# Kernel optimization log

Hardware: AMD Instinct MI355X
Metric: run time of the kernel (lower is better)

## Reference

```python
import jax, jax.numpy as jnp
import numpy as np

N = 4096      # nodes
IN = 512      # in_features
HEADS = 8
HPH = 8       # n_hidden // n_heads
HID = HEADS * HPH  # 64
CLS = 16      # n_classes
NEG_SLOPE = 0.2
MASK_VAL = -1e9


def setup_inputs() -> dict:
    key = jax.random.key(0)
    ks = jax.random.split(key, 8)
    x = jax.random.normal(ks[0], (N, IN), jnp.float32)
    # sparse-ish adjacency, avg degree ~16, with self loops
    adj = jax.random.bernoulli(ks[1], 16.0 / N, (N, N)) | jnp.eye(N, dtype=bool)
    W1 = jax.random.normal(ks[2], (IN, HEADS, HPH), jnp.float32) * 0.05
    a1l = jax.random.normal(ks[3], (HEADS, HPH), jnp.float32) * 0.05
    a1r = jax.random.normal(ks[4], (HEADS, HPH), jnp.float32) * 0.05
    W2 = jax.random.normal(ks[5], (HID, 1, CLS), jnp.float32) * 0.05
    a2l = jax.random.normal(ks[6], (1, CLS), jnp.float32) * 0.05
    a2r = jax.random.normal(ks[7], (1, CLS), jnp.float32) * 0.05
    return {"x": x, "adj": adj, "W1": W1, "a1l": a1l, "a1r": a1r,
            "W2": W2, "a2l": a2l, "a2r": a2r}


def gat_layer(x, adj, W, al, ar, is_concat):
    # project: [N, H, D]
    g = jnp.einsum('ni,ihd->nhd', x, W)
    # score e[i,j,h] = leaky_relu(a_l . g_i + a_r . g_j)
    sl = jnp.einsum('nhd,hd->nh', g, al)  # [N, H]
    sr = jnp.einsum('nhd,hd->nh', g, ar)  # [N, H]
    e = jax.nn.leaky_relu(sl[:, None, :] + sr[None, :, :], NEG_SLOPE)  # [N, N, H]
    e = jnp.where(adj[:, :, None], e, MASK_VAL)
    a = jax.nn.softmax(e, axis=1)                 # softmax over neighbors j
    out = jnp.einsum('ijh,jhd->ihd', a, g)        # [N, H, D]
    if is_concat:
        return out.reshape(out.shape[0], -1)      # [N, H*D]
    return out.mean(axis=1)                        # [N, D]


def reference(x, adj, W1, a1l, a1r, W2, a2l, a2r):
    # dropout layers are identity in eval mode
    h = gat_layer(x, adj, W1, a1l, a1r, True)   # [N, HID]
    h = jax.nn.elu(h)
    return gat_layer(h, adj, W2, a2l, a2r, False)  # [N, CLS]
```

## Files before the change

kernel.cpp:

```cpp
#include <hip/hip_runtime.h>
#include <hip/hip_bf16.h>

#define N_NODES 4096
#define IN_F 512
#define HEADS 8
#define HPH 8
#define HID 64
#define CLS 16
#define NEG_SLOPE 0.2f
#define MAXD 256
#define QCAP 256

__device__ __forceinline__ float leaky(float x) { return x > 0.f ? x : NEG_SLOPE * x; }

__global__ __launch_bounds__(256, 4) void scan_proj1(
        const int* __restrict__ adj,
        const float* __restrict__ x,
        const float* __restrict__ W1,
        const float* __restrict__ a1l,
        const float* __restrict__ a1r,
        float* __restrict__ g1,
        float* __restrict__ sl1,
        float* __restrict__ sr1,
        int* __restrict__ deg_g,
        int* __restrict__ nbr_g) {
    __shared__ float xs[16][516];
    __shared__ int wcnt[4];
    const int b = blockIdx.x;
    const int t = threadIdx.x;
    const int group = b / 17;
    const int role = b - group * 17;
    if (role < 16) {
        int* nbrS = (int*)&xs[0][0];
        const int w = t >> 6, lane = t & 63;
        const int i = group * 16 + role;
        const int4* q = (const int4*)(adj + (size_t)i * N_NODES) + w * 256;
        const int4 v0 = q[lane];
        const int4 v1 = q[lane + 64];
        const int4 v2 = q[lane + 128];
        const int4 v3 = q[lane + 192];
        const unsigned long long below = (1ull << lane) - 1ull;
        int* seg = nbrS + w * QCAP;
        const int jq = w * 1024;
        int segcnt = 0;
        {
            const int4 v = v0; const int s = 0;
            const bool fx = v.x != 0, fy = v.y != 0, fz = v.z != 0, fw = v.w != 0;
            const unsigned long long bx = __ballot(fx), by = __ballot(fy);
            const unsigned long long bz = __ballot(fz), bw = __ballot(fw);
            int base = segcnt + __popcll(bx & below) + __popcll(by & below)
                              + __popcll(bz & below) + __popcll(bw & below);
            const int j0 = jq + 4 * (lane + 64 * s);
            int r = 0;
            if (fx) { if (base + r < QCAP) seg[base + r] = j0;     ++r; }
            if (fy) { if (base + r < QCAP) seg[base + r] = j0 + 1; ++r; }
            if (fz) { if (base + r < QCAP) seg[base + r] = j0 + 2; ++r; }
            if (fw) { if (base + r < QCAP) seg[base + r] = j0 + 3; ++r; }
            segcnt += __popcll(bx) + __popcll(by) + __popcll(bz) + __popcll(bw);
        }
        {
            const int4 v = v1; const int s = 1;
            const bool fx = v.x != 0, fy = v.y != 0, fz = v.z != 0, fw = v.w != 0;
            const unsigned long long bx = __ballot(fx), by = __ballot(fy);
            const unsigned long long bz = __ballot(fz), bw = __ballot(fw);
            int base = segcnt + __popcll(bx & below) + __popcll(by & below)
                              + __popcll(bz & below) + __popcll(bw & below);
            const int j0 = jq + 4 * (lane + 64 * s);
            int r = 0;
            if (fx) { if (base + r < QCAP) seg[base + r] = j0;     ++r; }
            if (fy) { if (base + r < QCAP) seg[base + r] = j0 + 1; ++r; }
            if (fz) { if (base + r < QCAP) seg[base + r] = j0 + 2; ++r; }
            if (fw) { if (base + r < QCAP) seg[base + r] = j0 + 3; ++r; }
            segcnt += __popcll(bx) + __popcll(by) + __popcll(bz) + __popcll(bw);
        }
        {
            const int4 v = v2; const int s = 2;
            const bool fx = v.x != 0, fy = v.y != 0, fz = v.z != 0, fw = v.w != 0;
            const unsigned long long bx = __ballot(fx), by = __ballot(fy);
            const unsigned long long bz = __ballot(fz), bw = __ballot(fw);
            int base = segcnt + __popcll(bx & below) + __popcll(by & below)
                              + __popcll(bz & below) + __popcll(bw & below);
            const int j0 = jq + 4 * (lane + 64 * s);
            int r = 0;
            if (fx) { if (base + r < QCAP) seg[base + r] = j0;     ++r; }
            if (fy) { if (base + r < QCAP) seg[base + r] = j0 + 1; ++r; }
            if (fz) { if (base + r < QCAP) seg[base + r] = j0 + 2; ++r; }
            if (fw) { if (base + r < QCAP) seg[base + r] = j0 + 3; ++r; }
            segcnt += __popcll(bx) + __popcll(by) + __popcll(bz) + __popcll(bw);
        }
        {
            const int4 v = v3; const int s = 3;
            const bool fx = v.x != 0, fy = v.y != 0, fz = v.z != 0, fw = v.w != 0;
            const unsigned long long bx = __ballot(fx), by = __ballot(fy);
            const unsigned long long bz = __ballot(fz), bw = __ballot(fw);
            int base = segcnt + __popcll(bx & below) + __popcll(by & below)
                              + __popcll(bz & below) + __popcll(bw & below);
            const int j0 = jq + 4 * (lane + 64 * s);
            int r = 0;
            if (fx) { if (base + r < QCAP) seg[base + r] = j0;     ++r; }
            if (fy) { if (base + r < QCAP) seg[base + r] = j0 + 1; ++r; }
            if (fz) { if (base + r < QCAP) seg[base + r] = j0 + 2; ++r; }
            if (fw) { if (base + r < QCAP) seg[base + r] = j0 + 3; ++r; }
            segcnt += __popcll(bx) + __popcll(by) + __popcll(bz) + __popcll(bw);
        }
        const int myc = segcnt < QCAP ? segcnt : QCAP;
        if (lane == 0) wcnt[w] = myc;
        __syncthreads();
        const int off = (w > 0 ? wcnt[0] : 0) + (w > 1 ? wcnt[1] : 0)
                      + (w > 2 ? wcnt[2] : 0);
        const int total = wcnt[0] + wcnt[1] + wcnt[2] + wcnt[3];
        if (t == 0) deg_g[i] = total < MAXD ? total : MAXD;
        for (int k = lane; k < myc; k += 64) {
            const int pos = off + k;
            if (pos < MAXD) nbr_g[(size_t)i * MAXD + pos] = seg[k];
        }
        return;
    }
    const int i0 = group * 16;
    for (int l = t; l < 2048; l += 256) {
        const int r = l >> 7, c4 = l & 127;
        *(float4*)&xs[r][c4 * 4] = *(const float4*)(x + (size_t)(i0 + r) * IN_F + c4 * 4);
    }
    __syncthreads();
    const int wv = t >> 6;
    const int inner = t & 63;
    const int kq = inner >> 4;
    const int cg = inner & 15;
    float4 acc[4];
#pragma unroll
    for (int r = 0; r < 4; ++r) acc[r] = make_float4(0.f, 0.f, 0.f, 0.f);
    const float* xr[4];
#pragma unroll
    for (int r = 0; r < 4; ++r) xr[r] = &xs[wv * 4 + r][kq * 128];
    const float* Wq = W1 + (size_t)(kq * 128) * HID + cg * 4;
#pragma unroll 2
    for (int k = 0; k < 128; k += 4) {
        const float4 w0 = *(const float4*)(Wq + (size_t)(k + 0) * HID);
        const float4 w1 = *(const float4*)(Wq + (size_t)(k + 1) * HID);
        const float4 w2 = *(const float4*)(Wq + (size_t)(k + 2) * HID);
        const float4 w3 = *(const float4*)(Wq + (size_t)(k + 3) * HID);
#pragma unroll
        for (int r = 0; r < 4; ++r) {
            const float4 xv = *(const float4*)(xr[r] + k);
            acc[r].x += xv.x * w0.x + xv.y * w1.x + xv.z * w2.x + xv.w * w3.x;
            acc[r].y += xv.x * w0.y + xv.y * w1.y + xv.z * w2.y + xv.w * w3.y;
            acc[r].z += xv.x * w0.z + xv.y * w1.z + xv.z * w2.z + xv.w * w3.z;
            acc[r].w += xv.x * w0.w + xv.y * w1.w + xv.z * w2.w + xv.w * w3.w;
        }
    }
#pragma unroll
    for (int r = 0; r < 4; ++r) {
#pragma unroll
        for (int m = 16; m <= 32; m <<= 1) {
            acc[r].x += __shfl_xor(acc[r].x, m, 64);
            acc[r].y += __shfl_xor(acc[r].y, m, 64);
            acc[r].z += __shfl_xor(acc[r].z, m, 64);
            acc[r].w += __shfl_xor(acc[r].w, m, 64);
        }
    }
    if (kq == 0) {
        const float4 al = *(const float4*)(a1l + cg * 4);
        const float4 ar = *(const float4*)(a1r + cg * 4);
#pragma unroll
        for (int r = 0; r < 4; ++r) {
            const int i = i0 + wv * 4 + r;
            *(float4*)(g1 + (size_t)i * HID + cg * 4) = acc[r];
            float pl = acc[r].x * al.x + acc[r].y * al.y + acc[r].z * al.z + acc[r].w * al.w;
            float pr = acc[r].x * ar.x + acc[r].y * ar.y + acc[r].z * ar.z + acc[r].w * ar.w;
            pl += __shfl_xor(pl, 1, 64);
            pr += __shfl_xor(pr, 1, 64);
            if ((cg & 1) == 0) {
                sl1[i * HEADS + (cg >> 1)] = pl;
                sr1[i * HEADS + (cg >> 1)] = pr;
            }
        }
    }
}

__global__ __launch_bounds__(256) void attn1_fused(
        const float* __restrict__ g1,
        const float* __restrict__ sl1,
        const float* __restrict__ sr1,
        const float* __restrict__ W2,
        const float* __restrict__ a2l,
        const float* __restrict__ a2r,
        const int* __restrict__ deg_g,
        const int* __restrict__ nbr_g,
        float* __restrict__ g2,
        float* __restrict__ sl2,
        float* __restrict__ sr2) {
    const int w = threadIdx.x >> 6;
    const int t = threadIdx.x & 63;
    const int i = blockIdx.x * 4 + w;
    const int n = deg_g[i];
    const int jreg = nbr_g[(size_t)i * MAXD + t];
    const int h = t >> 3;
    const float sl = sl1[i * HEADS + h];
    float denom = 0.f, acc = 0.f;
    const int n64 = n < 64 ? n : 64;
    int k = 0;
    for (; k + 4 <= n64; k += 4) {
        const int j0 = __shfl(jreg, k),     j1 = __shfl(jreg, k + 1);
        const int j2 = __shfl(jreg, k + 2), j3 = __shfl(jreg, k + 3);
        const float s0 = sr1[j0 * HEADS + h], s1 = sr1[j1 * HEADS + h];
        const float s2 = sr1[j2 * HEADS + h], s3 = sr1[j3 * HEADS + h];
        const float v0 = g1[(size_t)j0 * HID + t], v1 = g1[(size_t)j1 * HID + t];
        const float v2 = g1[(size_t)j2 * HID + t], v3 = g1[(size_t)j3 * HID + t];
        const float w0 = __expf(leaky(sl + s0)), w1 = __expf(leaky(sl + s1));
        const float w2 = __expf(leaky(sl + s2)), w3 = __expf(leaky(sl + s3));
        denom += (w0 + w1) + (w2 + w3);
        acc += w0 * v0; acc += w1 * v1; acc += w2 * v2; acc += w3 * v3;
    }
    for (; k < n64; ++k) {
        const int jj = __shfl(jreg, k);
        const float wq = __expf(leaky(sl + sr1[jj * HEADS + h]));
        denom += wq;
        acc += wq * g1[(size_t)jj * HID + t];
    }
    for (; k < n; ++k) {
        const int jj = nbr_g[(size_t)i * MAXD + k];
        const float wq = __expf(leaky(sl + sr1[jj * HEADS + h]));
        denom += wq;
        acc += wq * g1[(size_t)jj * HID + t];
    }
    float o = (n > 0) ? (acc / denom) : 0.f;
    o = (o > 0.f) ? o : expm1f(o);
    const int q = t >> 4, c = t & 15;
    float p = 0.f;
#pragma unroll
    for (int kk = 0; kk < 16; ++kk) {
        const int k2 = q * 16 + kk;
        p += __shfl(o, k2) * W2[k2 * CLS + c];
    }
    p += __shfl_xor(p, 16, 64);
    p += __shfl_xor(p, 32, 64);
    float pl = 0.f, pr = 0.f;
    if (t < CLS) {
        g2[(size_t)i * CLS + t] = p;
        pl = p * a2l[t];
        pr = p * a2r[t];
    }
#pragma unroll
    for (int off = 1; off < 16; off <<= 1) {
        pl += __shfl_xor(pl, off, 64);
        pr += __shfl_xor(pr, off, 64);
    }
    if (t == 0) { sl2[i] = pl; sr2[i] = pr; }
}

__global__ __launch_bounds__(256) void attn2(
        const int* __restrict__ deg_g,
        const int* __restrict__ nbr_g,
        const float* __restrict__ g2,
        const float* __restrict__ sl2,
        const float* __restrict__ sr2,
        float* __restrict__ out) {
    const int w = threadIdx.x >> 6;
    const int t = threadIdx.x & 63;
    const int g = t >> 4;
    const int c = t & 15;
    const int node = blockIdx.x * 16 + w * 4 + g;
    const int n = deg_g[node];
    const int4 jv = *(const int4*)(nbr_g + (size_t)node * MAXD + 4 * c);
    const float sl = sl2[node];
    float denom = 0.f, acc = 0.f;
    const int n64 = n < 64 ? n : 64;
    int k = 0;
    for (; k + 4 <= n64; k += 4) {
        const int src = k >> 2;
        const int j0 = __shfl(jv.x, src, 16), j1 = __shfl(jv.y, src, 16);
        const int j2 = __shfl(jv.z, src, 16), j3 = __shfl(jv.w, src, 16);
        const float s0 = sr2[j0], s1 = sr2[j1], s2 = sr2[j2], s3 = sr2[j3];
        const float v0 = g2[(size_t)j0 * CLS + c], v1 = g2[(size_t)j1 * CLS + c];
        const float v2 = g2[(size_t)j2 * CLS + c], v3 = g2[(size_t)j3 * CLS + c];
        const float w0 = __expf(leaky(sl + s0)), w1 = __expf(leaky(sl + s1));
        const float w2 = __expf(leaky(sl + s2)), w3 = __expf(leaky(sl + s3));
        denom += (w0 + w1) + (w2 + w3);
        acc += w0 * v0; acc += w1 * v1; acc += w2 * v2; acc += w3 * v3;
    }
    for (; k < n64; ++k) {
        const int src = k >> 2, cm = k & 3;
        const int jx = __shfl(jv.x, src, 16), jy = __shfl(jv.y, src, 16);
        const int jz = __shfl(jv.z, src, 16), jw = __shfl(jv.w, src, 16);
        const int jj = cm == 0 ? jx : (cm == 1 ? jy : (cm == 2 ? jz : jw));
        const float wq = __expf(leaky(sl + sr2[jj]));
        denom += wq;
        acc += wq * g2[(size_t)jj * CLS + c];
    }
    for (; k < n; ++k) {
        const int jj = nbr_g[(size_t)node * MAXD + k];
        const float wq = __expf(leaky(sl + sr2[jj]));
        denom += wq;
        acc += wq * g2[(size_t)jj * CLS + c];
    }
    out[(size_t)node * CLS + c] = (n > 0) ? acc / denom : 0.f;
}

extern "C" void kernel_launch(void* const* d_in, const int* in_sizes, int n_in,
                              void* d_out, int out_size, void* d_ws, size_t ws_size,
                              hipStream_t stream) {
    const float* x   = (const float*)d_in[0];
    const int*   adj = (const int*)d_in[1];
    const float* W1  = (const float*)d_in[2];
    const float* a1l = (const float*)d_in[3];
    const float* a1r = (const float*)d_in[4];
    const float* W2  = (const float*)d_in[5];
    const float* a2l = (const float*)d_in[6];
    const float* a2r = (const float*)d_in[7];
    float* out = (float*)d_out;

    float* ws  = (float*)d_ws;
    float* g1  = ws;
    float* sl1 = g1  + (size_t)N_NODES * HID;
    float* sr1 = sl1 + (size_t)N_NODES * HEADS;
    float* g2  = sr1 + (size_t)N_NODES * HEADS;
    float* sl2 = g2  + (size_t)N_NODES * CLS;
    float* sr2 = sl2 + N_NODES;
    int*   deg = (int*)(sr2 + N_NODES);
    int*   nbr = deg + N_NODES;

    scan_proj1<<<17 * (N_NODES / 16), 256, 0, stream>>>(
        adj, x, W1, a1l, a1r, g1, sl1, sr1, deg, nbr);
    attn1_fused<<<N_NODES / 4, 256, 0, stream>>>(g1, sl1, sr1, W2, a2l, a2r,
                                                 deg, nbr, g2, sl2, sr2);
    attn2<<<N_NODES / 16, 256, 0, stream>>>(deg, nbr, g2, sl2, sr2, out);
}
```

Before: 131.1 us.

## Merge three kernels into one cooperative persistent kernel with grid syncs

Replaces the three separate launches (scan+projection, layer-1 attention, layer-2 attention) with one cooperative kernel. It loops over tasks with a grid-stride and separates the stages with grid-wide syncs. The aim is to remove kernel launch gaps and inter-kernel drain/fill overhead. In exchange the grid is capped by occupancy, grid syncs add latency, and the per-node work in each stage runs over fewer resident blocks.

```diff
diff --git a/kernel.cpp b/kernel.cpp
--- a/kernel.cpp
+++ b/kernel.cpp
@@ -1,5 +1,7 @@
 #include <hip/hip_runtime.h>
-#include <hip/hip_bf16.h>
+#include <hip/hip_cooperative_groups.h>
+
+namespace cg = cooperative_groups;
 
 #define N_NODES 4096
 #define IN_F 512
@@ -10,290 +12,241 @@
 #define NEG_SLOPE 0.2f
 #define MAXD 256
 #define QCAP 256
+#define TASKS (17 * (N_NODES / 16))
 
 __device__ __forceinline__ float leaky(float x) { return x > 0.f ? x : NEG_SLOPE * x; }
 
-__global__ __launch_bounds__(256, 4) void scan_proj1(
+__device__ __forceinline__ void emit4(int4 v, int j0, int* seg, int& segcnt,
+                                      unsigned long long below) {
+    const bool fx = v.x != 0, fy = v.y != 0, fz = v.z != 0, fw = v.w != 0;
+    const unsigned long long bx = __ballot(fx), by = __ballot(fy);
+    const unsigned long long bz = __ballot(fz), bw = __ballot(fw);
+    int base = segcnt + __popcll(bx & below) + __popcll(by & below)
+                      + __popcll(bz & below) + __popcll(bw & below);
+    int r = 0;
+    if (fx) { if (base + r < QCAP) seg[base + r] = j0;     ++r; }
+    if (fy) { if (base + r < QCAP) seg[base + r] = j0 + 1; ++r; }
+    if (fz) { if (base + r < QCAP) seg[base + r] = j0 + 2; ++r; }
+    if (fw) { if (base + r < QCAP) seg[base + r] = j0 + 3; ++r; }
+    segcnt += __popcll(bx) + __popcll(by) + __popcll(bz) + __popcll(bw);
+}
+
+__global__ __launch_bounds__(256, 4) void gat_all(
         const int* __restrict__ adj,
         const float* __restrict__ x,
         const float* __restrict__ W1,
         const float* __restrict__ a1l,
         const float* __restrict__ a1r,
+        const float* __restrict__ W2,
+        const float* __restrict__ a2l,
+        const float* __restrict__ a2r,
         float* __restrict__ g1,
         float* __restrict__ sl1,
         float* __restrict__ sr1,
+        float* __restrict__ g2,
+        float* __restrict__ sl2,
+        float* __restrict__ sr2,
         int* __restrict__ deg_g,
-        int* __restrict__ nbr_g) {
+        int* __restrict__ nbr_g,
+        float* __restrict__ out) {
     __shared__ float xs[16][516];
     __shared__ int wcnt[4];
-    const int b = blockIdx.x;
     const int t = threadIdx.x;
-    const int group = b / 17;
-    const int role = b - group * 17;
-    if (role < 16) {
-        int* nbrS = (int*)&xs[0][0];
-        const int w = t >> 6, lane = t & 63;
-        const int i = group * 16 + role;
-        const int4* q = (const int4*)(adj + (size_t)i * N_NODES) + w * 256;
-        const int4 v0 = q[lane];
-        const int4 v1 = q[lane + 64];
-        const int4 v2 = q[lane + 128];
-        const int4 v3 = q[lane + 192];
-        const unsigned long long below = (1ull << lane) - 1ull;
-        int* seg = nbrS + w * QCAP;
-        const int jq = w * 1024;
-        int segcnt = 0;
-        {
-            const int4 v = v0; const int s = 0;
-            const bool fx = v.x != 0, fy = v.y != 0, fz = v.z != 0, fw = v.w != 0;
-            const unsigned long long bx = __ballot(fx), by = __ballot(fy);
-            const unsigned long long bz = __ballot(fz), bw = __ballot(fw);
-            int base = segcnt + __popcll(bx & below) + __popcll(by & below)
-                              + __popcll(bz & below) + __popcll(bw & below);
-            const int j0 = jq + 4 * (lane + 64 * s);
-            int r = 0;
-            if (fx) { if (base + r < QCAP) seg[base + r] = j0;     ++r; }
-            if (fy) { if (base + r < QCAP) seg[base + r] = j0 + 1; ++r; }
-            if (fz) { if (base + r < QCAP) seg[base + r] = j0 + 2; ++r; }
-            if (fw) { if (base + r < QCAP) seg[base + r] = j0 + 3; ++r; }
-            segcnt += __popcll(bx) + __popcll(by) + __popcll(bz) + __popcll(bw);
-        }
-        {
-            const int4 v = v1; const int s = 1;
-            const bool fx = v.x != 0, fy = v.y != 0, fz = v.z != 0, fw = v.w != 0;
-            const unsigned long long bx = __ballot(fx), by = __ballot(fy);
-            const unsigned long long bz = __ballot(fz), bw = __ballot(fw);
-            int base = segcnt + __popcll(bx & below) + __popcll(by & below)
-                              + __popcll(bz & below) + __popcll(bw & below);
-            const int j0 = jq + 4 * (lane + 64 * s);
-            int r = 0;
-            if (fx) { if (base + r < QCAP) seg[base + r] = j0;     ++r; }
-            if (fy) { if (base + r < QCAP) seg[base + r] = j0 + 1; ++r; }
-            if (fz) { if (base + r < QCAP) seg[base + r] = j0 + 2; ++r; }
-            if (fw) { if (base + r < QCAP) seg[base + r] = j0 + 3; ++r; }
-            segcnt += __popcll(bx) + __popcll(by) + __popcll(bz) + __popcll(bw);
-        }
-        {
-            const int4 v = v2; const int s = 2;
-            const bool fx = v.x != 0, fy = v.y != 0, fz = v.z != 0, fw = v.w != 0;
-            const unsigned long long bx = __ballot(fx), by = __ballot(fy);
-            const unsigned long long bz = __ballot(fz), bw = __ballot(fw);
-            int base = segcnt + __popcll(bx & below) + __popcll(by & below)
-                              + __popcll(bz & below) + __popcll(bw & below);
-            const int j0 = jq + 4 * (lane + 64 * s);
-            int r = 0;
-            if (fx) { if (base + r < QCAP) seg[base + r] = j0;     ++r; }
-            if (fy) { if (base + r < QCAP) seg[base + r] = j0 + 1; ++r; }
-            if (fz) { if (base + r < QCAP) seg[base + r] = j0 + 2; ++r; }
-            if (fw) { if (base + r < QCAP) seg[base + r] = j0 + 3; ++r; }
-            segcnt += __popcll(bx) + __popcll(by) + __popcll(bz) + __popcll(bw);
-        }
-        {
-            const int4 v = v3; const int s = 3;
-            const bool fx = v.x != 0, fy = v.y != 0, fz = v.z != 0, fw = v.w != 0;
-            const unsigned long long bx = __ballot(fx), by = __ballot(fy);
-            const unsigned long long bz = __ballot(fz), bw = __ballot(fw);
-            int base = segcnt + __popcll(bx & below) + __popcll(by & below)
-                              + __popcll(bz & below) + __popcll(bw & below);
-            const int j0 = jq + 4 * (lane + 64 * s);
-            int r = 0;
-            if (fx) { if (base + r < QCAP) seg[base + r] = j0;     ++r; }
-            if (fy) { if (base + r < QCAP) seg[base + r] = j0 + 1; ++r; }
-            if (fz) { if (base + r < QCAP) seg[base + r] = j0 + 2; ++r; }
-            if (fw) { if (base + r < QCAP) seg[base + r] = j0 + 3; ++r; }
-            segcnt += __popcll(bx) + __popcll(by) + __popcll(bz) + __popcll(bw);
-        }
-        const int myc = segcnt < QCAP ? segcnt : QCAP;
-        if (lane == 0) wcnt[w] = myc;
+    const int w = t >> 6, lane = t & 63;
+
+    for (int task = blockIdx.x; task < TASKS; task += gridDim.x) {
         __syncthreads();
-        const int off = (w > 0 ? wcnt[0] : 0) + (w > 1 ? wcnt[1] : 0)
-                      + (w > 2 ? wcnt[2] : 0);
-        const int total = wcnt[0] + wcnt[1] + wcnt[2] + wcnt[3];
-        if (t == 0) deg_g[i] = total < MAXD ? total : MAXD;
-        for (int k = lane; k < myc; k += 64) {
-            const int pos = off + k;
-            if (pos < MAXD) nbr_g[(size_t)i * MAXD + pos] = seg[k];
-        }
-        return;
-    }
-    const int i0 = group * 16;
-    for (int l = t; l < 2048; l += 256) {
-        const int r = l >> 7, c4 = l & 127;
-        *(float4*)&xs[r][c4 * 4] = *(const float4*)(x + (size_t)(i0 + r) * IN_F + c4 * 4);
-    }
-    __syncthreads();
-    const int wv = t >> 6;
-    const int inner = t & 63;
-    const int kq = inner >> 4;
-    const int cg = inner & 15;
-    float4 acc[4];
-#pragma unroll
-    for (int r = 0; r < 4; ++r) acc[r] = make_float4(0.f, 0.f, 0.f, 0.f);
-    const float* xr[4];
-#pragma unroll
-    for (int r = 0; r < 4; ++r) xr[r] = &xs[wv * 4 + r][kq * 128];
-    const float* Wq = W1 + (size_t)(kq * 128) * HID + cg * 4;
+        const int group = task / 17;
+        const int role = task - group * 17;
+        if (role < 16) {
+            int* nbrS = (int*)&xs[0][0];
+            const int i = group * 16 + role;
+            const int4* q = (const int4*)(adj + (size_t)i * N_NODES) + w * 256;
+            const int4 v0 = q[lane];
+            const int4 v1 = q[lane + 64];
+            const int4 v2 = q[lane + 128];
+            const int4 v3 = q[lane + 192];
+            const unsigned long long below = (1ull << lane) - 1ull;
+            int* seg = nbrS + w * QCAP;
+            const int jq = w * 1024;
+            int segcnt = 0;
+            emit4(v0, jq + 4 * lane, seg, segcnt, below);
+            emit4(v1, jq + 4 * (lane + 64), seg, segcnt, below);
+            emit4(v2, jq + 4 * (lane + 128), seg, segcnt, below);
+            emit4(v3, jq + 4 * (lane + 192), seg, segcnt, below);
+            const int myc = segcnt < QCAP ? segcnt : QCAP;
+            if (lane == 0) wcnt[w] = myc;
+            __syncthreads();
+            const int off = (w > 0 ? wcnt[0] : 0) + (w > 1 ? wcnt[1] : 0)
+                          + (w > 2 ? wcnt[2] : 0);
+            const int total = wcnt[0] + wcnt[1] + wcnt[2] + wcnt[3];
+            if (t == 0) deg_g[i] = total < MAXD ? total : MAXD;
+            for (int k = lane; k < myc; k += 64) {
+                const int pos = off + k;
+                if (pos < MAXD) nbr_g[(size_t)i * MAXD + pos] = seg[k];
+            }
+        } else {
+            const int i0 = group * 16;
+            for (int l = t; l < 2048; l += 256) {
+                const int r = l >> 7, c4 = l & 127;
+                *(float4*)&xs[r][c4 * 4] =
+                    *(const float4*)(x + (size_t)(i0 + r) * IN_F + c4 * 4);
+            }
+            __syncthreads();
+            const int kq = lane >> 4;
+            const int cg = lane & 15;
+            float4 acc[4];
+#pragma unroll
+            for (int r = 0; r < 4; ++r) acc[r] = make_float4(0.f, 0.f, 0.f, 0.f);
+            const float* xr[4];
+#pragma unroll
+            for (int r = 0; r < 4; ++r) xr[r] = &xs[w * 4 + r][kq * 128];
+            const float* Wq = W1 + (size_t)(kq * 128) * HID + cg * 4;
 #pragma unroll 2
-    for (int k = 0; k < 128; k += 4) {
-        const float4 w0 = *(const float4*)(Wq + (size_t)(k + 0) * HID);
-        const float4 w1 = *(const float4*)(Wq + (size_t)(k + 1) * HID);
-        const float4 w2 = *(const float4*)(Wq + (size_t)(k + 2) * HID);
-        const float4 w3 = *(const float4*)(Wq + (size_t)(k + 3) * HID);
-#pragma unroll
-        for (int r = 0; r < 4; ++r) {
-            const float4 xv = *(const float4*)(xr[r] + k);
-            acc[r].x += xv.x * w0.x + xv.y * w1.x + xv.z * w2.x + xv.w * w3.x;
-            acc[r].y += xv.x * w0.y + xv.y * w1.y + xv.z * w2.y + xv.w * w3.y;
-            acc[r].z += xv.x * w0.z + xv.y * w1.z + xv.z * w2.z + xv.w * w3.z;
-            acc[r].w += xv.x * w0.w + xv.y * w1.w + xv.z * w2.w + xv.w * w3.w;
-        }
-    }
-#pragma unroll
-    for (int r = 0; r < 4; ++r) {
-#pragma unroll
-        for (int m = 16; m <= 32; m <<= 1) {
-            acc[r].x += __shfl_xor(acc[r].x, m, 64);
-            acc[r].y += __shfl_xor(acc[r].y, m, 64);
-            acc[r].z += __shfl_xor(acc[r].z, m, 64);
-            acc[r].w += __shfl_xor(acc[r].w, m, 64);
-        }
-    }
-    if (kq == 0) {
-        const float4 al = *(const float4*)(a1l + cg * 4);
-        const float4 ar = *(const float4*)(a1r + cg * 4);
-#pragma unroll
-        for (int r = 0; r < 4; ++r) {
-            const int i = i0 + wv * 4 + r;
-            *(float4*)(g1 + (size_t)i * HID + cg * 4) = acc[r];
-            float pl = acc[r].x * al.x + acc[r].y * al.y + acc[r].z * al.z + acc[r].w * al.w;
-            float pr = acc[r].x * ar.x + acc[r].y * ar.y + acc[r].z * ar.z + acc[r].w * ar.w;
-            pl += __shfl_xor(pl, 1, 64);
-            pr += __shfl_xor(pr, 1, 64);
-            if ((cg & 1) == 0) {
-                sl1[i * HEADS + (cg >> 1)] = pl;
-                sr1[i * HEADS + (cg >> 1)] = pr;
-            }
-        }
-    }
-}
-
-__global__ __launch_bounds__(256) void attn1_fused(
-        const float* __restrict__ g1,
-        const float* __restrict__ sl1,
-        const float* __restrict__ sr1,
-        const float* __restrict__ W2,
-        const float* __restrict__ a2l,
-        const float* __restrict__ a2r,
-        const int* __restrict__ deg_g,
-        const int* __restrict__ nbr_g,
-        float* __restrict__ g2,
-        float* __restrict__ sl2,
-        float* __restrict__ sr2) {
-    const int w = threadIdx.x >> 6;
-    const int t = threadIdx.x & 63;
-    const int i = blockIdx.x * 4 + w;
-    const int n = deg_g[i];
-    const int jreg = nbr_g[(size_t)i * MAXD + t];
-    const int h = t >> 3;
-    const float sl = sl1[i * HEADS + h];
-    float denom = 0.f, acc = 0.f;
-    const int n64 = n < 64 ? n : 64;
-    int k = 0;
-    for (; k + 4 <= n64; k += 4) {
-        const int j0 = __shfl(jreg, k),     j1 = __shfl(jreg, k + 1);
-        const int j2 = __shfl(jreg, k + 2), j3 = __shfl(jreg, k + 3);
-        const float s0 = sr1[j0 * HEADS + h], s1 = sr1[j1 * HEADS + h];
-        const float s2 = sr1[j2 * HEADS + h], s3 = sr1[j3 * HEADS + h];
-        const float v0 = g1[(size_t)j0 * HID + t], v1 = g1[(size_t)j1 * HID + t];
-        const float v2 = g1[(size_t)j2 * HID + t], v3 = g1[(size_t)j3 * HID + t];
-        const float w0 = __expf(leaky(sl + s0)), w1 = __expf(leaky(sl + s1));
-        const float w2 = __expf(leaky(sl + s2)), w3 = __expf(leaky(sl + s3));
-        denom += (w0 + w1) + (w2 + w3);
-        acc += w0 * v0; acc += w1 * v1; acc += w2 * v2; acc += w3 * v3;
-    }
-    for (; k < n64; ++k) {
-        const int jj = __shfl(jreg, k);
-        const float wq = __expf(leaky(sl + sr1[jj * HEADS + h]));
-        denom += wq;
-        acc += wq * g1[(size_t)jj * HID + t];
-    }
-    for (; k < n; ++k) {
-        const int jj = nbr_g[(size_t)i * MAXD + k];
-        const float wq = __expf(leaky(sl + sr1[jj * HEADS + h]));
-        denom += wq;
-        acc += wq * g1[(size_t)jj * HID + t];
-    }
-    float o = (n > 0) ? (acc / denom) : 0.f;
-    o = (o > 0.f) ? o : expm1f(o);
-    const int q = t >> 4, c = t & 15;
-    float p = 0.f;
-#pragma unroll
-    for (int kk = 0; kk < 16; ++kk) {
-        const int k2 = q * 16 + kk;
-        p += __shfl(o, k2) * W2[k2 * CLS + c];
-    }
-    p += __shfl_xor(p, 16, 64);
-    p += __shfl_xor(p, 32, 64);
-    float pl = 0.f, pr = 0.f;
-    if (t < CLS) {
-        g2[(size_t)i * CLS + t] = p;
-        pl = p * a2l[t];
-        pr = p * a2r[t];
-    }
-#pragma unroll
-    for (int off = 1; off < 16; off <<= 1) {
-        pl += __shfl_xor(pl, off, 64);
-        pr += __shfl_xor(pr, off, 64);
-    }
-    if (t == 0) { sl2[i] = pl; sr2[i] = pr; }
-}
-
-__global__ __launch_bounds__(256) void attn2(
-        const int* __restrict__ deg_g,
-        const int* __restrict__ nbr_g,
-        const float* __restrict__ g2,
-        const float* __restrict__ sl2,
-        const float* __restrict__ sr2,
-        float* __restrict__ out) {
-    const int w = threadIdx.x >> 6;
-    const int t = threadIdx.x & 63;
-    const int g = t >> 4;
-    const int c = t & 15;
-    const int node = blockIdx.x * 16 + w * 4 + g;
-    const int n = deg_g[node];
-    const int4 jv = *(const int4*)(nbr_g + (size_t)node * MAXD + 4 * c);
-    const float sl = sl2[node];
-    float denom = 0.f, acc = 0.f;
-    const int n64 = n < 64 ? n : 64;
-    int k = 0;
-    for (; k + 4 <= n64; k += 4) {
-        const int src = k >> 2;
-        const int j0 = __shfl(jv.x, src, 16), j1 = __shfl(jv.y, src, 16);
-        const int j2 = __shfl(jv.z, src, 16), j3 = __shfl(jv.w, src, 16);
-        const float s0 = sr2[j0], s1 = sr2[j1], s2 = sr2[j2], s3 = sr2[j3];
-        const float v0 = g2[(size_t)j0 * CLS + c], v1 = g2[(size_t)j1 * CLS + c];
-        const float v2 = g2[(size_t)j2 * CLS + c], v3 = g2[(size_t)j3 * CLS + c];
-        const float w0 = __expf(leaky(sl + s0)), w1 = __expf(leaky(sl + s1));
-        const float w2 = __expf(leaky(sl + s2)), w3 = __expf(leaky(sl + s3));
-        denom += (w0 + w1) + (w2 + w3);
-        acc += w0 * v0; acc += w1 * v1; acc += w2 * v2; acc += w3 * v3;
-    }
-    for (; k < n64; ++k) {
-        const int src = k >> 2, cm = k & 3;
-        const int jx = __shfl(jv.x, src, 16), jy = __shfl(jv.y, src, 16);
-        const int jz = __shfl(jv.z, src, 16), jw = __shfl(jv.w, src, 16);
-        const int jj = cm == 0 ? jx : (cm == 1 ? jy : (cm == 2 ? jz : jw));
-        const float wq = __expf(leaky(sl + sr2[jj]));
-        denom += wq;
-        acc += wq * g2[(size_t)jj * CLS + c];
-    }
-    for (; k < n; ++k) {
-        const int jj = nbr_g[(size_t)node * MAXD + k];
-        const float wq = __expf(leaky(sl + sr2[jj]));
-        denom += wq;
-        acc += wq * g2[(size_t)jj * CLS + c];
-    }
-    out[(size_t)node * CLS + c] = (n > 0) ? acc / denom : 0.f;
+            for (int k = 0; k < 128; k += 4) {
+                const float4 w0 = *(const float4*)(Wq + (size_t)(k + 0) * HID);
+                const float4 w1 = *(const float4*)(Wq + (size_t)(k + 1) * HID);
+                const float4 w2 = *(const float4*)(Wq + (size_t)(k + 2) * HID);
+                const float4 w3 = *(const float4*)(Wq + (size_t)(k + 3) * HID);
+#pragma unroll
+                for (int r = 0; r < 4; ++r) {
+                    const float4 xv = *(const float4*)(xr[r] + k);
+                    acc[r].x += xv.x * w0.x + xv.y * w1.x + xv.z * w2.x + xv.w * w3.x;
+                    acc[r].y += xv.x * w0.y + xv.y * w1.y + xv.z * w2.y + xv.w * w3.y;
+                    acc[r].z += xv.x * w0.z + xv.y * w1.z + xv.z * w2.z + xv.w * w3.z;
+                    acc[r].w += xv.x * w0.w + xv.y * w1.w + xv.z * w2.w + xv.w * w3.w;
+                }
+            }
+#pragma unroll
+            for (int r = 0; r < 4; ++r) {
+#pragma unroll
+                for (int m = 16; m <= 32; m <<= 1) {
+                    acc[r].x += __shfl_xor(acc[r].x, m, 64);
+                    acc[r].y += __shfl_xor(acc[r].y, m, 64);
+                    acc[r].z += __shfl_xor(acc[r].z, m, 64);
+                    acc[r].w += __shfl_xor(acc[r].w, m, 64);
+                }
+            }
+            if (kq == 0) {
+                const float4 al = *(const float4*)(a1l + cg * 4);
+                const float4 ar = *(const float4*)(a1r + cg * 4);
+#pragma unroll
+                for (int r = 0; r < 4; ++r) {
+                    const int i = i0 + w * 4 + r;
+                    *(float4*)(g1 + (size_t)i * HID + cg * 4) = acc[r];
+                    float pl = acc[r].x * al.x + acc[r].y * al.y + acc[r].z * al.z + acc[r].w * al.w;
+                    float pr = acc[r].x * ar.x + acc[r].y * ar.y + acc[r].z * ar.z + acc[r].w * ar.w;
+                    pl += __shfl_xor(pl, 1, 64);
+                    pr += __shfl_xor(pr, 1, 64);
+                    if ((cg & 1) == 0) {
+                        sl1[i * HEADS + (cg >> 1)] = pl;
+                        sr1[i * HEADS + (cg >> 1)] = pr;
+                    }
+                }
+            }
+        }
+    }
+    __threadfence();
+    cg::this_grid().sync();
+    __threadfence();
+
+    for (int i = blockIdx.x * 4 + w; i < N_NODES; i += gridDim.x * 4) {
+        const int n = deg_g[i];
+        const int jreg = nbr_g[(size_t)i * MAXD + lane];
+        const int h = lane >> 3;
+        const float sl = sl1[i * HEADS + h];
+        float denom = 0.f, acc = 0.f;
+        const int n64 = n < 64 ? n : 64;
+        int k = 0;
+        for (; k + 4 <= n64; k += 4) {
+            const int j0 = __shfl(jreg, k),     j1 = __shfl(jreg, k + 1);
+            const int j2 = __shfl(jreg, k + 2), j3 = __shfl(jreg, k + 3);
+            const float s0 = sr1[j0 * HEADS + h], s1 = sr1[j1 * HEADS + h];
+            const float s2 = sr1[j2 * HEADS + h], s3 = sr1[j3 * HEADS + h];
+            const float v0 = g1[(size_t)j0 * HID + lane], v1 = g1[(size_t)j1 * HID + lane];
+            const float v2 = g1[(size_t)j2 * HID + lane], v3 = g1[(size_t)j3 * HID + lane];
+            const float w0 = __expf(leaky(sl + s0)), w1 = __expf(leaky(sl + s1));
+            const float w2 = __expf(leaky(sl + s2)), w3 = __expf(leaky(sl + s3));
+            denom += (w0 + w1) + (w2 + w3);
+            acc += w0 * v0; acc += w1 * v1; acc += w2 * v2; acc += w3 * v3;
+        }
+        for (; k < n64; ++k) {
+            const int jj = __shfl(jreg, k);
+            const float wq = __expf(leaky(sl + sr1[jj * HEADS + h]));
+            denom += wq;
+            acc += wq * g1[(size_t)jj * HID + lane];
+        }
+        for (; k < n; ++k) {
+            const int jj = nbr_g[(size_t)i * MAXD + k];
+            const float wq = __expf(leaky(sl + sr1[jj * HEADS + h]));
+            denom += wq;
+            acc += wq * g1[(size_t)jj * HID + lane];
+        }
+        float o = (n > 0) ? (acc / denom) : 0.f;
+        o = (o > 0.f) ? o : expm1f(o);
+        const int q = lane >> 4, c = lane & 15;
+        float p = 0.f;
+#pragma unroll
+        for (int kk = 0; kk < 16; ++kk) {
+            const int k2 = q * 16 + kk;
+            p += __shfl(o, k2) * W2[k2 * CLS + c];
+        }
+        p += __shfl_xor(p, 16, 64);
+        p += __shfl_xor(p, 32, 64);
+        float pl = 0.f, pr = 0.f;
+        if (lane < CLS) {
+            g2[(size_t)i * CLS + lane] = p;
+            pl = p * a2l[lane];
+            pr = p * a2r[lane];
+        }
+#pragma unroll
+        for (int off = 1; off < 16; off <<= 1) {
+            pl += __shfl_xor(pl, off, 64);
+            pr += __shfl_xor(pr, off, 64);
+        }
+        if (lane == 0) { sl2[i] = pl; sr2[i] = pr; }
+    }
+    __threadfence();
+    cg::this_grid().sync();
+    __threadfence();
+
+    for (int node = blockIdx.x * 4 + w; node < N_NODES; node += gridDim.x * 4) {
+        const int c = lane & 15;
+        const int n = deg_g[node];
+        const int4 jv = *(const int4*)(nbr_g + (size_t)node * MAXD + 4 * c);
+        const float sl = sl2[node];
+        float denom = 0.f, acc = 0.f;
+        const int n64 = n < 64 ? n : 64;
+        int k = 0;
+        for (; k + 4 <= n64; k += 4) {
+            const int src = k >> 2;
+            const int j0 = __shfl(jv.x, src, 16), j1 = __shfl(jv.y, src, 16);
+            const int j2 = __shfl(jv.z, src, 16), j3 = __shfl(jv.w, src, 16);
+            const float s0 = sr2[j0], s1 = sr2[j1], s2 = sr2[j2], s3 = sr2[j3];
+            const float v0 = g2[(size_t)j0 * CLS + c], v1 = g2[(size_t)j1 * CLS + c];
+            const float v2 = g2[(size_t)j2 * CLS + c], v3 = g2[(size_t)j3 * CLS + c];
+            const float w0 = __expf(leaky(sl + s0)), w1 = __expf(leaky(sl + s1));
+            const float w2 = __expf(leaky(sl + s2)), w3 = __expf(leaky(sl + s3));
+            denom += (w0 + w1) + (w2 + w3);
+            acc += w0 * v0; acc += w1 * v1; acc += w2 * v2; acc += w3 * v3;
+        }
+        for (; k < n64; ++k) {
+            const int src = k >> 2, cm = k & 3;
+            const int jx = __shfl(jv.x, src, 16), jy = __shfl(jv.y, src, 16);
+            const int jz = __shfl(jv.z, src, 16), jw = __shfl(jv.w, src, 16);
+            const int jj = cm == 0 ? jx : (cm == 1 ? jy : (cm == 2 ? jz : jw));
+            const float wq = __expf(leaky(sl + sr2[jj]));
+            denom += wq;
+            acc += wq * g2[(size_t)jj * CLS + c];
+        }
+        for (; k < n; ++k) {
+            const int jj = nbr_g[(size_t)node * MAXD + k];
+            const float wq = __expf(leaky(sl + sr2[jj]));
+            denom += wq;
+            acc += wq * g2[(size_t)jj * CLS + c];
+        }
+        if (lane < 16) out[(size_t)node * CLS + c] = (n > 0) ? acc / denom : 0.f;
+    }
 }
 
 extern "C" void kernel_launch(void* const* d_in, const int* in_sizes, int n_in,
@@ -319,9 +272,21 @@
     int*   deg = (int*)(sr2 + N_NODES);
     int*   nbr = deg + N_NODES;
 
-    scan_proj1<<<17 * (N_NODES / 16), 256, 0, stream>>>(
-        adj, x, W1, a1l, a1r, g1, sl1, sr1, deg, nbr);
-    attn1_fused<<<N_NODES / 4, 256, 0, stream>>>(g1, sl1, sr1, W2, a2l, a2r,
-                                                 deg, nbr, g2, sl2, sr2);
-    attn2<<<N_NODES / 16, 256, 0, stream>>>(deg, nbr, g2, sl2, sr2, out);
+    static int grid = 0;
+    if (grid == 0) {
+        int per_cu = 0;
+        if (hipOccupancyMaxActiveBlocksPerMultiprocessor(&per_cu, gat_all, 256, 0)
+                != hipSuccess || per_cu < 1)
+            per_cu = 1;
+        grid = per_cu * 256;
+        if (grid > 1024) grid = 1024;
+    }
+
+    void* args[] = {(void*)&adj, (void*)&x, (void*)&W1, (void*)&a1l, (void*)&a1r,
+                    (void*)&W2, (void*)&a2l, (void*)&a2r,
+                    (void*)&g1, (void*)&sl1, (void*)&sr1,
+                    (void*)&g2, (void*)&sl2, (void*)&sr2,
+                    (void*)&deg, (void*)&nbr, (void*)&out};
+    hipLaunchCooperativeKernel((void*)gat_all, dim3(grid), dim3(256),
+                               args, 0, stream);
 }
```

New measurement: 424.0 us. 3.23x slower.
